# Optimization experiments

Hardware: AMD Instinct MI355X
Metric: run time of the kernel (lower is better)

The kernel has to match this reference:

```python
import jax, jax.numpy as jnp
import numpy as np


def _affine_mats(thetas, lambda1s, lambda2s, H, W):
    # Replicates torch.stack(rows, dim=1) then stack(dim=2): the 'rows' end up as COLUMNS,
    # exactly matching the original module's construction.
    z = jnp.zeros_like(lambda1s)
    o = jnp.ones_like(lambda1s)
    scale = jnp.stack([jnp.stack([lambda1s, z, z], 1),
                       jnp.stack([z, lambda2s, z], 1),
                       jnp.stack([z, z, o], 1)], axis=2)  # [B,3,3]
    th = -thetas
    rot = jnp.stack([jnp.stack([jnp.cos(th), jnp.sin(th), z], 1),
                     jnp.stack([-jnp.sin(th), jnp.cos(th), z], 1),
                     jnp.stack([z, z, o], 1)], axis=2)
    trans = jnp.stack([jnp.stack([o, z, o * W], 1),
                       jnp.stack([z, o, o * H], 1),
                       jnp.stack([z, z, o], 1)], axis=2)
    fw = rot @ trans                       # forward_warp
    fws = scale @ fw                       # forward_warp_scaled
    overall = jnp.linalg.inv(jnp.linalg.inv(fw) @ fws)
    return overall[:, 0:2, :]              # [B,2,3]


def _affine_grid(theta, H, W):
    # torch affine_grid, align_corners=False: normalized pixel-center coords in [-1,1]
    xs = (jnp.arange(W, dtype=theta.dtype) + 0.5) * (2.0 / W) - 1.0
    ys = (jnp.arange(H, dtype=theta.dtype) + 0.5) * (2.0 / H) - 1.0
    X, Y = jnp.meshgrid(xs, ys)                        # [H,W]
    base = jnp.stack([X, Y, jnp.ones_like(X)], -1)     # [H,W,3]
    return jnp.einsum('bij,hwj->bhwi', theta, base)    # [B,H,W,2] (x,y)


def _grid_sample_bilinear_zeros(x, grid):
    # torch grid_sample(mode='bilinear', padding_mode='zeros', align_corners=False)
    B, C, H, W = x.shape
    gx = (grid[..., 0] + 1.0) * (W * 0.5) - 0.5        # [B,H,W] source pixel coords
    gy = (grid[..., 1] + 1.0) * (H * 0.5) - 0.5
    x0 = jnp.floor(gx); y0 = jnp.floor(gy)
    x1 = x0 + 1.0;      y1 = y0 + 1.0
    wx1 = gx - x0; wx0 = 1.0 - wx1
    wy1 = gy - y0; wy0 = 1.0 - wy1
    x0i = x0.astype(jnp.int32); x1i = x1.astype(jnp.int32)
    y0i = y0.astype(jnp.int32); y1i = y1.astype(jnp.int32)
    b_idx = jnp.arange(B)[:, None, None]

    def gather(yi, xi):
        yc = jnp.clip(yi, 0, H - 1)
        xc = jnp.clip(xi, 0, W - 1)
        v = x[b_idx, :, yc, xc]                        # [B,H,W,C]
        m = ((yi >= 0) & (yi < H) & (xi >= 0) & (xi < W)).astype(x.dtype)
        return v * m[..., None]

    out = (gather(y0i, x0i) * (wy0 * wx0)[..., None]
           + gather(y0i, x1i) * (wy0 * wx1)[..., None]
           + gather(y1i, x0i) * (wy1 * wx0)[..., None]
           + gather(y1i, x1i) * (wy1 * wx1)[..., None])  # [B,H,W,C]
    return jnp.transpose(out, (0, 3, 1, 2))            # [B,C,H,W]


def setup_inputs() -> dict:
    key = jax.random.key(0)
    k1, k2, k3, k4 = jax.random.split(key, 4)
    B, C, H, W = 32, 3, 512, 512
    return {
        'x': jax.random.normal(k1, (B, C, H, W), dtype=jnp.float32),
        'thetas': jax.random.normal(k2, (B,), dtype=jnp.float32),
        'lambda1s': jax.random.uniform(k3, (B,), dtype=jnp.float32),
        'lambda2s': jax.random.uniform(k4, (B,), dtype=jnp.float32),
    }


def reference(x, thetas, lambda1s, lambda2s):
    H, W = x.shape[2], x.shape[3]
    theta = _affine_mats(thetas, lambda1s, lambda2s, H, W)   # [B,2,3]
    grid = _affine_grid(theta, H, W)                         # [B,H,W,2]
    return _grid_sample_bilinear_zeros(x, grid).astype(jnp.float32)
```

## Files before the change

kernel.cpp:

```cpp
#include <hip/hip_runtime.h>
#include <math.h>

constexpr int B = 32;
constexpr int C = 3;
constexpr int H = 512;
constexpr int W = 512;
constexpr int HW = H * W;

__global__ __launch_bounds__(256)
void warp_kernel(const float* __restrict__ x,
                 const float* __restrict__ thetas,
                 const float* __restrict__ l1s,
                 const float* __restrict__ l2s,
                 float* __restrict__ out) {
    const int b = blockIdx.y;

    __shared__ float sc[4];
    if (threadIdx.x == 0) {
        double th = -(double)thetas[b];
        double c = cos(th), s = sin(th);
        double a = 1.0 / (double)l1s[b];
        double d = 1.0 / (double)l2s[b];
        sc[0] = (float)(a * c * c + d * s * s);
        sc[1] = (float)(c * s * (d - a));
        sc[2] = sc[1];
        sc[3] = (float)(a * s * s + d * c * c);
    }
    __syncthreads();
    const float t00 = sc[0], t01 = sc[1], t10 = sc[2], t11 = sc[3];

    const int tid   = threadIdx.x;
    const int lane  = tid & 63;
    const int wv    = tid >> 6;
    const int h     = (blockIdx.x << 1) | (wv >> 1);
    const int wbase = (wv & 1) << 8;

    const float Y = ((float)h + 0.5f) * (2.0f / (float)H) - 1.0f;

    int   xb[4], row0[4], row1[4];
    bool  xeq[4], vx0[4], vx1[4], pr0[4], pr1[4];
    float w00[4], w01[4], w10[4], w11[4];
    bool any_valid = false;

    #pragma unroll
    for (int j = 0; j < 4; ++j) {
        const int w = wbase + (j << 6) + lane;
        const float X = ((float)w + 0.5f) * (2.0f / (float)W) - 1.0f;
        const float gx = (t00 * X + t01 * Y + 1.0f) * ((float)W * 0.5f) - 0.5f;
        const float gy = (t10 * X + t11 * Y + 1.0f) * ((float)H * 0.5f) - 0.5f;

        const float x0f = floorf(gx), y0f = floorf(gy);
        const float wx1 = gx - x0f, wx0 = 1.0f - wx1;
        const float wy1 = gy - y0f, wy0 = 1.0f - wy1;

        const int x0 = (int)x0f, y0 = (int)y0f;
        const int x1 = x0 + 1,  y1 = y0 + 1;

        vx0[j] = ((unsigned)x0 < (unsigned)W);
        vx1[j] = ((unsigned)x1 < (unsigned)W);
        const bool vy0 = ((unsigned)y0 < (unsigned)H);
        const bool vy1 = ((unsigned)y1 < (unsigned)H);

        const int xbj = min(max(x0, 0), W - 2);
        xb[j]  = xbj;
        xeq[j] = (x0 == xbj);
        const bool anyx = vx0[j] || vx1[j];
        pr0[j] = vy0 && anyx;
        pr1[j] = vy1 && anyx;
        any_valid = any_valid || pr0[j] || pr1[j];

        row0[j] = min(max(y0, 0), H - 1) * W + xbj;
        row1[j] = min(max(y1, 0), H - 1) * W + xbj;

        w00[j] = wy0 * wx0; w01[j] = wy0 * wx1;
        w10[j] = wy1 * wx0; w11[j] = wy1 * wx1;
    }

    float r[C][4];
    #pragma unroll
    for (int ch = 0; ch < C; ++ch)
        #pragma unroll
        for (int j = 0; j < 4; ++j) r[ch][j] = 0.0f;

    if (any_valid) {
        const float* __restrict__ base = x + (size_t)b * C * HW;
        #pragma unroll
        for (int j = 0; j < 4; ++j) {
            #pragma unroll
            for (int ch = 0; ch < C; ++ch) {
                const float* __restrict__ p = base + ch * HW;
                float2 a0 = make_float2(0.0f, 0.0f);
                float2 a1 = make_float2(0.0f, 0.0f);
                if (pr0[j]) a0 = *reinterpret_cast<const float2*>(p + row0[j]);
                if (pr1[j]) a1 = *reinterpret_cast<const float2*>(p + row1[j]);
                const float v00 = vx0[j] ? (xeq[j] ? a0.x : a0.y) : 0.0f;
                const float v01 = vx1[j] ? (xeq[j] ? a0.y : a0.x) : 0.0f;
                const float v10 = vx0[j] ? (xeq[j] ? a1.x : a1.y) : 0.0f;
                const float v11 = vx1[j] ? (xeq[j] ? a1.y : a1.x) : 0.0f;
                r[ch][j] = v00 * w00[j] + v01 * w01[j] + v10 * w10[j] + v11 * w11[j];
            }
        }
    }

    const size_t obase = (size_t)b * C * HW + (size_t)h * W + (size_t)wbase + lane;
    #pragma unroll
    for (int ch = 0; ch < C; ++ch) {
        #pragma unroll
        for (int j = 0; j < 4; ++j) {
            out[obase + (size_t)ch * HW + (j << 6)] = r[ch][j];
        }
    }
}

extern "C" void kernel_launch(void* const* d_in, const int* in_sizes, int n_in,
                              void* d_out, int out_size, void* d_ws, size_t ws_size,
                              hipStream_t stream) {
    const float* x      = (const float*)d_in[0];
    const float* thetas = (const float*)d_in[1];
    const float* l1s    = (const float*)d_in[2];
    const float* l2s    = (const float*)d_in[3];
    float* out          = (float*)d_out;

    warp_kernel<<<dim3(H / 2, B), 256, 0, stream>>>(x, thetas, l1s, l2s, out);
}
```

Baseline: 188.5 us.

## Remap blocks per XCD, fold validity into weights, batch loads, nontemporal stores

The grid becomes 1D and is remapped so that each XCD (block index mod 8) handles whole batch images, which keeps one image's source data in the same L2. Boundary validity now zeroes the bilinear weights, so the loads run unconditionally from clamped addresses. All channel loads for a pixel group are issued before any math, giving more memory parallelism. Output writes use nontemporal stores to avoid polluting the cache. Loads now always happen, even for out-of-range taps, which can add traffic when much of the output falls outside the source image.

Result: slower. 204.6 us (+8.5%).

```diff
diff --git a/kernel.cpp b/kernel.cpp
--- a/kernel.cpp
+++ b/kernel.cpp
@@ -13,7 +13,11 @@
                  const float* __restrict__ l1s,
                  const float* __restrict__ l2s,
                  float* __restrict__ out) {
-    const int b = blockIdx.y;
+    const int lid  = blockIdx.x;
+    const int xcd  = lid & 7;
+    const int slot = lid >> 3;
+    const int b    = xcd + ((slot >> 8) << 3);
+    const int hb   = slot & 255;
 
     __shared__ float sc[4];
     if (threadIdx.x == 0) {
@@ -32,13 +36,13 @@
     const int tid   = threadIdx.x;
     const int lane  = tid & 63;
     const int wv    = tid >> 6;
-    const int h     = (blockIdx.x << 1) | (wv >> 1);
+    const int h     = (hb << 1) | (wv >> 1);
     const int wbase = (wv & 1) << 8;
 
     const float Y = ((float)h + 0.5f) * (2.0f / (float)H) - 1.0f;
 
-    int   xb[4], row0[4], row1[4];
-    bool  xeq[4], vx0[4], vx1[4], pr0[4], pr1[4];
+    int   row0[4], row1[4];
+    bool  xeq[4];
     float w00[4], w01[4], w10[4], w11[4];
     bool any_valid = false;
 
@@ -56,24 +60,23 @@
         const int x0 = (int)x0f, y0 = (int)y0f;
         const int x1 = x0 + 1,  y1 = y0 + 1;
 
-        vx0[j] = ((unsigned)x0 < (unsigned)W);
-        vx1[j] = ((unsigned)x1 < (unsigned)W);
+        const bool vx0 = ((unsigned)x0 < (unsigned)W);
+        const bool vx1 = ((unsigned)x1 < (unsigned)W);
         const bool vy0 = ((unsigned)y0 < (unsigned)H);
         const bool vy1 = ((unsigned)y1 < (unsigned)H);
 
         const int xbj = min(max(x0, 0), W - 2);
-        xb[j]  = xbj;
         xeq[j] = (x0 == xbj);
-        const bool anyx = vx0[j] || vx1[j];
-        pr0[j] = vy0 && anyx;
-        pr1[j] = vy1 && anyx;
-        any_valid = any_valid || pr0[j] || pr1[j];
 
         row0[j] = min(max(y0, 0), H - 1) * W + xbj;
         row1[j] = min(max(y1, 0), H - 1) * W + xbj;
 
-        w00[j] = wy0 * wx0; w01[j] = wy0 * wx1;
-        w10[j] = wy1 * wx0; w11[j] = wy1 * wx1;
+        w00[j] = (vy0 && vx0) ? wy0 * wx0 : 0.0f;
+        w01[j] = (vy0 && vx1) ? wy0 * wx1 : 0.0f;
+        w10[j] = (vy1 && vx0) ? wy1 * wx0 : 0.0f;
+        w11[j] = (vy1 && vx1) ? wy1 * wx1 : 0.0f;
+
+        any_valid = any_valid || ((vy0 || vy1) && (vx0 || vx1));
     }
 
     float r[C][4];
@@ -86,17 +89,18 @@
         const float* __restrict__ base = x + (size_t)b * C * HW;
         #pragma unroll
         for (int j = 0; j < 4; ++j) {
+            float2 a0[C], a1[C];
             #pragma unroll
             for (int ch = 0; ch < C; ++ch) {
-                const float* __restrict__ p = base + ch * HW;
-                float2 a0 = make_float2(0.0f, 0.0f);
-                float2 a1 = make_float2(0.0f, 0.0f);
-                if (pr0[j]) a0 = *reinterpret_cast<const float2*>(p + row0[j]);
-                if (pr1[j]) a1 = *reinterpret_cast<const float2*>(p + row1[j]);
-                const float v00 = vx0[j] ? (xeq[j] ? a0.x : a0.y) : 0.0f;
-                const float v01 = vx1[j] ? (xeq[j] ? a0.y : a0.x) : 0.0f;
-                const float v10 = vx0[j] ? (xeq[j] ? a1.x : a1.y) : 0.0f;
-                const float v11 = vx1[j] ? (xeq[j] ? a1.y : a1.x) : 0.0f;
+                a0[ch] = *reinterpret_cast<const float2*>(base + ch * HW + row0[j]);
+                a1[ch] = *reinterpret_cast<const float2*>(base + ch * HW + row1[j]);
+            }
+            #pragma unroll
+            for (int ch = 0; ch < C; ++ch) {
+                const float v00 = xeq[j] ? a0[ch].x : a0[ch].y;
+                const float v01 = xeq[j] ? a0[ch].y : a0[ch].x;
+                const float v10 = xeq[j] ? a1[ch].x : a1[ch].y;
+                const float v11 = xeq[j] ? a1[ch].y : a1[ch].x;
                 r[ch][j] = v00 * w00[j] + v01 * w01[j] + v10 * w10[j] + v11 * w11[j];
             }
         }
@@ -107,7 +111,8 @@
     for (int ch = 0; ch < C; ++ch) {
         #pragma unroll
         for (int j = 0; j < 4; ++j) {
-            out[obase + (size_t)ch * HW + (j << 6)] = r[ch][j];
+            __builtin_nontemporal_store(r[ch][j],
+                                        out + obase + (size_t)ch * HW + (j << 6));
         }
     }
 }
@@ -121,5 +126,5 @@
     const float* l2s    = (const float*)d_in[3];
     float* out          = (float*)d_out;
 
-    warp_kernel<<<dim3(H / 2, B), 256, 0, stream>>>(x, thetas, l1s, l2s, out);
+    warp_kernel<<<dim3((H / 2) * B), 256, 0, stream>>>(x, thetas, l1s, l2s, out);
 }
```
